# Kernel optimization log

Measured on AMD Instinct MI355X. Metric: run time of the kernel, lower is better.

Reference implementation:

```python
import jax, jax.numpy as jnp
import numpy as np

D_MODEL, N_HEADS, N_LEVELS, N_POINTS = 256, 8, 3, 4
HW = [(100, 152), (50, 76), (25, 38)]
S_TOTAL = sum(h * w for h, w in HW)  # 19950
B = 4


def _bilinear_sample(img, gx, gy, H, W):
    # img: [N, H*W, D]; gx, gy: [N, M] normalized coords in [-1, 1]
    # grid_sample semantics: align_corners=False, padding_mode='zeros'
    ix = (gx + 1.0) * 0.5 * W - 0.5
    iy = (gy + 1.0) * 0.5 * H - 0.5
    x0 = jnp.floor(ix)
    y0 = jnp.floor(iy)
    wx1 = ix - x0
    wy1 = iy - y0

    def corner(xc, yc, w):
        valid = (xc >= 0) & (xc < W) & (yc >= 0) & (yc < H)
        idx = (jnp.clip(yc, 0, H - 1) * W + jnp.clip(xc, 0, W - 1)).astype(jnp.int32)
        vals = jnp.take_along_axis(img, idx[:, :, None], axis=1)  # [N, M, D]
        return vals * (w * valid.astype(img.dtype))[:, :, None]

    return (corner(x0, y0, (1 - wx1) * (1 - wy1))
            + corner(x0 + 1, y0, wx1 * (1 - wy1))
            + corner(x0, y0 + 1, (1 - wx1) * wy1)
            + corner(x0 + 1, y0 + 1, wx1 * wy1))


def setup_inputs() -> dict:
    key = jax.random.key(0)
    ks = jax.random.split(key, 10)
    C = D_MODEL
    sc = 1.0 / np.sqrt(C)
    query = jax.random.normal(ks[0], (B, S_TOTAL, C), jnp.float32)
    value = jax.random.normal(ks[1], (B, S_TOTAL, C), jnp.float32)
    reference_points = jax.random.uniform(ks[2], (B, S_TOTAL, 2), jnp.float32)
    spatial_shapes = np.array(HW, dtype=np.int64)
    sizes = [h * w for h, w in HW]
    level_start_index = np.concatenate([[0], np.cumsum(sizes)[:-1]]).astype(np.int64)
    # Small offset weights keep sampled locations mostly in-bounds (as after training)
    W_off = jax.random.normal(ks[3], (N_HEADS * N_LEVELS * N_POINTS * 2, C), jnp.float32) * 0.01
    b_off = jax.random.normal(ks[4], (N_HEADS * N_LEVELS * N_POINTS * 2,), jnp.float32)
    W_attn = jax.random.normal(ks[5], (N_HEADS * N_LEVELS * N_POINTS, C), jnp.float32) * sc
    b_attn = jnp.zeros((N_HEADS * N_LEVELS * N_POINTS,), jnp.float32)
    W_val = jax.random.normal(ks[6], (C, C), jnp.float32) * sc
    b_val = jnp.zeros((C,), jnp.float32)
    W_out = jax.random.normal(ks[7], (C, C), jnp.float32) * sc
    b_out = jnp.zeros((C,), jnp.float32)
    return {"query": query, "value": value, "spatial_shapes": spatial_shapes,
            "level_start_index": level_start_index, "reference_points": reference_points,
            "W_off": W_off, "b_off": b_off, "W_attn": W_attn, "b_attn": b_attn,
            "W_val": W_val, "b_val": b_val, "W_out": W_out, "b_out": b_out}


def reference(query, value, spatial_shapes, level_start_index, reference_points,
              W_off, b_off, W_attn, b_attn, W_val, b_val, W_out, b_out):
    Bq, S, C = query.shape
    Dh = C // N_HEADS
    ss = np.asarray(spatial_shapes)          # static [L,2] (H,W)
    lsi = np.asarray(level_start_index)      # static [L]

    v = (value @ W_val.T + b_val).reshape(Bq, S, N_HEADS, Dh)
    off = (query @ W_off.T + b_off).reshape(Bq, S, N_HEADS, N_LEVELS, N_POINTS, 2)
    attn = jax.nn.softmax(
        (query @ W_attn.T + b_attn).reshape(Bq, S, N_HEADS, N_LEVELS, N_POINTS), axis=-1)

    # normalizer per level: (W, H) to normalize (x, y) offsets
    normalizer = jnp.asarray(ss[:, ::-1].astype(np.float32))  # [L, 2]
    ref = reference_points[:, :, None, None, None, :]          # [B,S,1,1,1,2]
    loc = ref + off / normalizer[None, None, None, :, None, :]  # [B,S,H,L,P,2]

    out = jnp.zeros((Bq, S, N_HEADS, Dh), query.dtype)
    for lvl in range(N_LEVELS):
        H, W = int(ss[lvl, 0]), int(ss[lvl, 1])
        start = int(lsi[lvl])
        # value for this level: [B*Hn, H*W, Dh]
        v_l = v[:, start:start + H * W].transpose(0, 2, 1, 3).reshape(Bq * N_HEADS, H * W, Dh)
        g = loc[:, :, :, lvl] * 2.0 - 1.0                      # [B,S,Hn,P,2]
        g = g.transpose(0, 2, 1, 3, 4).reshape(Bq * N_HEADS, S * N_POINTS, 2)
        sampled = _bilinear_sample(v_l, g[..., 0], g[..., 1], H, W)  # [B*Hn, S*P, Dh]
        sampled = sampled.reshape(Bq, N_HEADS, S, N_POINTS, Dh)
        w_l = attn[:, :, :, lvl].transpose(0, 2, 1, 3)         # [B,Hn,S,P]
        out = out + jnp.einsum('bhspd,bhsp->bshd', sampled, w_l)
    return out.reshape(Bq, S, C) @ W_out.T + b_out
```

## Files before the change

kernel.cpp:

```cpp
#include <hip/hip_runtime.h>

typedef unsigned short u16;
typedef unsigned int u32;
typedef __attribute__((ext_vector_type(8))) short short8v;
typedef __attribute__((ext_vector_type(4))) float f32x4;
typedef __attribute__((ext_vector_type(2))) float f32x2;
typedef __attribute__((ext_vector_type(4))) unsigned int uint4v;
typedef __attribute__((ext_vector_type(2))) unsigned int uint2v;
typedef __attribute__((ext_vector_type(8))) unsigned short us8;
typedef __attribute__((ext_vector_type(4))) unsigned short us4;

#define B_   4
#define S_   19950
#define C_   256
#define NH   8
#define DH   32
#define BS_  (B_*S_)

#define BM 64
#define BN 128
#define BK 64
#define NPAN 1248

__device__ __forceinline__ float bf2f(u16 u){ u32 x=((u32)u)<<16; float f; __builtin_memcpy(&f,&x,4); return f; }
__device__ __forceinline__ u16 f2bf(float f){ u32 x; __builtin_memcpy(&x,&f,4); x += 0x7fffu + ((x>>16)&1u); return (u16)(x>>16); }
__device__ __forceinline__ u32 cvtpk(float a, float b){ u32 r; asm("v_cvt_pk_bf16_f32 %0, %1, %2" : "=v"(r) : "v"(a), "v"(b)); return r; }
__device__ __forceinline__ f32x2 pkfma(f32x2 a, f32x2 b, f32x2 d){
  asm("v_pk_fma_f32 %0, %1, %2, %0" : "+v"(d) : "v"(a), "v"(b)); return d;
}
__device__ __forceinline__ f32x2 unpk(u32 p){
  uint2v u; u.x = p<<16; u.y = p & 0xffff0000u; return __builtin_bit_cast(f32x2, u);
}

template<int MODE>
__device__ __forceinline__ void gemm_core(int g, u32* smem,
    const void* __restrict__ Aany, const float* __restrict__ Wmain,
    const float* __restrict__ Wattn, const float* __restrict__ bmain,
    const float* __restrict__ battn, void* __restrict__ out0, u16* __restrict__ out1)
{
  constexpr int NX = (MODE==1) ? 3 : 2;
  float* Asf = (float*)smem;
  u16*  Asb  = (u16*)smem;
  u32*  Bs   = smem + ((MODE==2) ? 2048 : 4096);

  const int tid = threadIdx.x;
  const int x = (g>>3) % NX;
  const int y = ((g>>3)/NX)*8 + (g&7);
  const int m0 = y * BM;
  const int n0 = x * BN;
  const int lane = tid & 63;
  const int wid  = tid >> 6;
  const int wm = wid >> 1, wn = wid & 1;
  const int ln15 = lane & 15, ln4 = lane >> 4;

  f32x4 acc[2][4];
  #pragma unroll
  for (int i=0;i<2;++i){
    #pragma unroll
    for (int j=0;j<4;++j) acc[i][j] = (f32x4){0.f,0.f,0.f,0.f};
  }

  f32x4 bvv[8];
  auto loadB = [&](int k0){
    #pragma unroll
    for (int i=0;i<8;++i){
      const int ct = tid + 256*i;
      const int row = ct >> 4, c = ct & 15;
      const int n = n0 + row;
      f32x4 vv = (f32x4){0.f,0.f,0.f,0.f};
      if constexpr (MODE==1) {
        if (n < 192)      vv = *(const f32x4*)(Wmain + (size_t)n*C_ + k0 + c*4);
        else if (n < 288) vv = *(const f32x4*)(Wattn + (size_t)(n-192)*C_ + k0 + c*4);
      } else {
        vv = *(const f32x4*)(Wmain + (size_t)n*C_ + k0 + c*4);
      }
      bvv[i] = vv;
    }
  };

  loadB(0);

  #pragma unroll
  for (int kt=0; kt<4; ++kt) {
    const int k0 = kt*BK;
    if constexpr (MODE==2) {
      const u16* Ab = (const u16*)Aany;
      #pragma unroll
      for (int i=0;i<2;++i){
        const int rl = wid*16 + i*8 + (lane>>3);
        const int rg = min(m0 + rl, BS_-1);
        const int c = lane & 7, cs = c ^ (rl & 7);
        __builtin_amdgcn_global_load_lds(Ab + (size_t)rg*C_ + k0 + cs*8,
            &Asb[(wid*16 + i*8)*64], 16, 0, 0);
      }
    } else {
      const float* Ab = (const float*)Aany;
      #pragma unroll
      for (int i=0;i<4;++i){
        const int rl = wid*16 + i*4 + (lane>>4);
        const int rg = min(m0 + rl, BS_-1);
        const int c = lane & 15, cs = c ^ (rl & 15);
        __builtin_amdgcn_global_load_lds(Ab + (size_t)rg*C_ + k0 + cs*4,
            &Asf[(wid*16 + i*4)*64], 16, 0, 0);
      }
    }
    #pragma unroll
    for (int i=0;i<8;++i){
      const int ct = tid + 256*i;
      const int row = ct >> 4, c = ct & 15;
      const u32 p0 = cvtpk(bvv[i].x, bvv[i].y), p1 = cvtpk(bvv[i].z, bvv[i].w);
      const int cc = c >> 1;
      uint2v pk; pk.x = p0; pk.y = p1;
      *(uint2v*)&Bs[row*32 + ((cc ^ (row&7))<<2) + (c&1)*2] = pk;
    }
    if (kt < 3) loadB(k0 + BK);
    __syncthreads();
    #pragma unroll
    for (int ks=0; ks<2; ++ks) {
      short8v af[2], bfr[4];
      #pragma unroll
      for (int mi=0;mi<2;++mi){
        const int row = wm*32 + mi*16 + ln15;
        if constexpr (MODE==2) {
          const int c = ks*4 + ln4;
          af[mi] = *(const short8v*)&Asb[row*64 + ((c ^ (row&7))<<3)];
        } else {
          const int ch = ks*8 + ln4*2;
          const int c1 = ch ^ (row&15), c2 = (ch+1) ^ (row&15);
          const f32x4 lo = *(const f32x4*)&Asf[row*64 + c1*4];
          const f32x4 hi = *(const f32x4*)&Asf[row*64 + c2*4];
          uint4v uu;
          uu.x = cvtpk(lo.x, lo.y); uu.y = cvtpk(lo.z, lo.w);
          uu.z = cvtpk(hi.x, hi.y); uu.w = cvtpk(hi.z, hi.w);
          af[mi] = __builtin_bit_cast(short8v, uu);
        }
      }
      #pragma unroll
      for (int ni=0;ni<4;++ni){
        const int row = wn*64 + ni*16 + ln15;
        const int c = ks*4 + ln4;
        bfr[ni] = *(const short8v*)&Bs[row*32 + ((c ^ (row&7))<<2)];
      }
      #pragma unroll
      for (int mi=0;mi<2;++mi){
        #pragma unroll
        for (int ni=0;ni<4;++ni)
          acc[mi][ni] = __builtin_amdgcn_mfma_f32_16x16x32_bf16(af[mi], bfr[ni], acc[mi][ni], 0, 0, 0);
      }
    }
    __syncthreads();
  }

  if constexpr (MODE==2) {
    float* Cs = (float*)smem;
    float* outp = (float*)out0;
    #pragma unroll
    for (int p=0;p<2;++p){
      if (wm == p) {
        #pragma unroll
        for (int mi=0;mi<2;++mi){
          #pragma unroll
          for (int ni=0;ni<4;++ni){
            const int col = wn*64 + ni*16 + ln15;
            const float bv = bmain[n0 + col];
            #pragma unroll
            for (int j=0;j<4;++j){
              const int rl = mi*16 + ln4*4 + j;
              Cs[rl*132 + col] = acc[mi][ni][j] + bv;
            }
          }
        }
      }
      __syncthreads();
      #pragma unroll
      for (int i=0;i<4;++i){
        const int c = i*256 + tid;
        const int row = c >> 5, ch = c & 31;
        const int m = m0 + p*32 + row;
        if (m < BS_) {
          const f32x4 vv = *(const f32x4*)&Cs[row*132 + ch*4];
          *(f32x4*)(outp + (size_t)m*C_ + n0 + ch*4) = vv;
        }
      }
      __syncthreads();
    }
  } else {
    u16* Cs = (u16*)smem;
    #pragma unroll
    for (int mi=0;mi<2;++mi){
      #pragma unroll
      for (int ni=0;ni<4;++ni){
        const int col = wn*64 + ni*16 + ln15;
        const int n = n0 + col;
        if (MODE==1 && n >= 288) continue;
        float bias;
        if constexpr (MODE==1) bias = (n < 192) ? bmain[n] : battn[n-192];
        else                   bias = bmain[n];
        if (MODE==1 && n >= 192) {
          #pragma unroll
          for (int j=0;j<4;++j){
            const int row = wm*32 + mi*16 + ln4*4 + j;
            const float vv = acc[mi][ni][j] + bias;
            float mx = vv;
            mx = fmaxf(mx, __shfl_xor(mx, 1));
            mx = fmaxf(mx, __shfl_xor(mx, 2));
            const float e = __expf(vv - mx);
            float ssum = e;
            ssum += __shfl_xor(ssum, 1);
            ssum += __shfl_xor(ssum, 2);
            Cs[row*136 + col] = f2bf(e/ssum);
          }
        } else {
          #pragma unroll
          for (int j=0;j<4;++j){
            const int row = wm*32 + mi*16 + ln4*4 + j;
            Cs[row*136 + col] = f2bf(acc[mi][ni][j] + bias);
          }
        }
      }
    }
    __syncthreads();
    #pragma unroll
    for (int i=0;i<4;++i){
      const int c = i*256 + tid;
      const int row = c >> 4, ch = c & 15;
      const int m = m0 + row;
      if (m >= BS_) continue;
      const int colg = n0 + ch*8;
      const int bq = m / S_, sq = m - bq*S_;
      if constexpr (MODE==0) {
        const uint4v vv = *(const uint4v*)&Cs[row*136 + ch*8];
        u16* vout = (u16*)out0;
        const int h = colg >> 5, dh0 = colg & 31;
        *(uint4v*)(vout + ((size_t)(bq*NH+h)*S_ + sq)*DH + dh0) = vv;
      } else {
        if (colg < 192) {
          const uint4v vv = *(const uint4v*)&Cs[row*136 + ch*8];
          u16* soff = (u16*)out0;
          const int hh = colg / 24, cc = colg - hh*24;
          *(uint4v*)(soff + (((size_t)hh*4 + bq)*S_ + sq)*24 + cc) = vv;
        } else if (colg < 288) {
          #pragma unroll
          for (int half=0; half<2; ++half){
            const int nl2 = colg + half*4 - 192;
            const int hh = nl2 / 12, cc = nl2 - hh*12;
            const uint2v vv = *(const uint2v*)&Cs[row*136 + ch*8 + half*4];
            *(uint2v*)(out1 + (((size_t)hh*4 + bq)*S_ + sq)*12 + cc) = vv;
          }
        }
      }
    }
  }
}

__global__ __launch_bounds__(256) void k_projF(
    const void* __restrict__ value, const float* __restrict__ Wv,
    const float* __restrict__ bv, void* __restrict__ vout,
    const void* __restrict__ query, const float* __restrict__ Wo,
    const float* __restrict__ Wa, const float* __restrict__ bo,
    const float* __restrict__ ba, void* __restrict__ soff, u16* __restrict__ sattn)
{
  __shared__ u32 smem[8192];
  const int g = blockIdx.x;
  if (g < 2*NPAN) gemm_core<0>(g,          smem, value, Wv, nullptr, bv, nullptr, vout, nullptr);
  else            gemm_core<1>(g - 2*NPAN, smem, query, Wo, Wa,      bo, ba,      soff, sattn);
}

__global__ __launch_bounds__(256) void k_gemm2F(const void* __restrict__ A,
    const float* __restrict__ W, const float* __restrict__ b, void* __restrict__ o)
{
  __shared__ u32 smem[6144];
  gemm_core<2>(blockIdx.x, smem, A, W, nullptr, b, nullptr, o, nullptr);
}

#define NCH 312

__global__ __launch_bounds__(256) void k_sample7(const u16* __restrict__ v,
    const u16* __restrict__ soff, const u16* __restrict__ sattn,
    const float* __restrict__ refp, u16* __restrict__ tmp)
{
  const int g = blockIdx.x;
  const int xcd = g & 7, inner = g >> 3;
  const int unit = inner / NCH;
  const int cidx = inner - unit*NCH;
  const int bh = xcd*4 + unit;
  const int b = bh >> 3, h = bh & 7;
  const int dh0 = (threadIdx.x & 3) * 8;
  const int q = cidx*64 + (threadIdx.x >> 2);
  if (q >= S_) return;
  const size_t r = (size_t)b*S_ + q;
  const float refx = refp[r*2+0], refy = refp[r*2+1];
  const char* vb = (const char*)(v + (size_t)bh * S_ * DH);

  const u16* sop = soff + (((size_t)h*4 + b)*S_ + q)*24;
  const u16* sap = sattn + (((size_t)h*4 + b)*S_ + q)*12;
  us8 so0 = *(const us8*)(sop);
  us8 so1 = *(const us8*)(sop + 8);
  us8 so2 = *(const us8*)(sop + 16);
  us4 sa0 = *(const us4*)(sap);
  us4 sa1 = *(const us4*)(sap + 4);
  us4 sa2 = *(const us4*)(sap + 8);
  u16 soarr[24]; u16 saarr[12];
  #pragma unroll
  for (int i=0;i<8;++i){ soarr[i]=so0[i]; soarr[8+i]=so1[i]; soarr[16+i]=so2[i]; }
  #pragma unroll
  for (int i=0;i<4;++i){ saarr[i]=sa0[i]; saarr[4+i]=sa1[i]; saarr[8+i]=sa2[i]; }

  f32x2 acc0 = (f32x2){0.f,0.f}, acc1 = acc0, acc2 = acc0, acc3 = acc0;
  const int WLs[3]={152,76,38}, HLs[3]={100,50,25}, STs[3]={0,15200,19000};
  const u32 ch2 = (u32)(dh0*2);
  #pragma unroll
  for (int l=0;l<3;++l) {
    const int Wl=WLs[l], Hl=HLs[l];
    const float rxl = refx*(float)Wl - 0.5f;
    const float ryl = refy*(float)Hl - 0.5f;
    const char* vbl = vb + (size_t)STs[l]*DH*2;
    #pragma unroll
    for (int p=0;p<4;++p) {
      const int idx = l*4 + p;
      const float ix = rxl + bf2f(soarr[2*idx+0]);
      const float iy = ryl + bf2f(soarr[2*idx+1]);
      const float aw = bf2f(saarr[idx]);
      const float x0f = floorf(ix), y0f = floorf(iy);
      const float wx1 = ix-x0f, wy1 = iy-y0f;
      const int x0 = (int)x0f, y0 = (int)y0f;
      const int x1 = x0+1, y1 = y0+1;
      const float wx0z = ((u32)x0 < (u32)Wl) ? (1.f-wx1) : 0.f;
      const float wx1z = ((u32)x1 < (u32)Wl) ? wx1 : 0.f;
      const float wy0z = ((u32)y0 < (u32)Hl) ? aw*(1.f-wy1) : 0.f;
      const float wy1z = ((u32)y1 < (u32)Hl) ? aw*wy1 : 0.f;
      const int xi0 = min(max(x0,0),Wl-1), xi1 = min(max(x1,0),Wl-1);
      const int yi0 = min(max(y0,0),Hl-1), yi1 = min(max(y1,0),Hl-1);
      const u32 rb0 = (u32)(yi0*Wl)*64u + ch2;
      const u32 rb1 = (u32)(yi1*Wl)*64u + ch2;
      const uint4v t00 = *(const uint4v*)(vbl + rb0 + (u32)xi0*64u);
      const uint4v t01 = *(const uint4v*)(vbl + rb0 + (u32)xi1*64u);
      const uint4v t10 = *(const uint4v*)(vbl + rb1 + (u32)xi0*64u);
      const uint4v t11 = *(const uint4v*)(vbl + rb1 + (u32)xi1*64u);
      const float w00 = wx0z*wy0z, w01 = wx1z*wy0z;
      const float w10 = wx0z*wy1z, w11 = wx1z*wy1z;
      f32x2 W00 = (f32x2){w00,w00}, W01 = (f32x2){w01,w01};
      f32x2 W10 = (f32x2){w10,w10}, W11 = (f32x2){w11,w11};
      acc0 = pkfma(unpk(t00.x), W00, acc0);
      acc1 = pkfma(unpk(t00.y), W00, acc1);
      acc2 = pkfma(unpk(t00.z), W00, acc2);
      acc3 = pkfma(unpk(t00.w), W00, acc3);
      acc0 = pkfma(unpk(t01.x), W01, acc0);
      acc1 = pkfma(unpk(t01.y), W01, acc1);
      acc2 = pkfma(unpk(t01.z), W01, acc2);
      acc3 = pkfma(unpk(t01.w), W01, acc3);
      acc0 = pkfma(unpk(t10.x), W10, acc0);
      acc1 = pkfma(unpk(t10.y), W10, acc1);
      acc2 = pkfma(unpk(t10.z), W10, acc2);
      acc3 = pkfma(unpk(t10.w), W10, acc3);
      acc0 = pkfma(unpk(t11.x), W11, acc0);
      acc1 = pkfma(unpk(t11.y), W11, acc1);
      acc2 = pkfma(unpk(t11.z), W11, acc2);
      acc3 = pkfma(unpk(t11.w), W11, acc3);
    }
  }
  uint4v o;
  o.x = cvtpk(acc0.x, acc0.y); o.y = cvtpk(acc1.x, acc1.y);
  o.z = cvtpk(acc2.x, acc2.y); o.w = cvtpk(acc3.x, acc3.y);
  *(uint4v*)(tmp + r*C_ + (size_t)h*DH + dh0) = o;
}

extern "C" void kernel_launch(void* const* d_in, const int* in_sizes, int n_in,
                              void* d_out, int out_size, void* d_ws, size_t ws_size,
                              hipStream_t stream) {
  (void)in_sizes; (void)n_in; (void)out_size; (void)ws_size;
  const float* query = (const float*)d_in[0];
  const float* value = (const float*)d_in[1];
  const float* refp  = (const float*)d_in[4];
  const float* W_off = (const float*)d_in[5];
  const float* b_off = (const float*)d_in[6];
  const float* W_attn= (const float*)d_in[7];
  const float* b_attn= (const float*)d_in[8];
  const float* W_val = (const float*)d_in[9];
  const float* b_val = (const float*)d_in[10];
  const float* W_out = (const float*)d_in[11];
  const float* b_out = (const float*)d_in[12];
  float* out = (float*)d_out;

  char* ws = (char*)d_ws;
  constexpr size_t V_BYTES    = (size_t)BS_*C_*2;
  constexpr size_t SOFF_BYTES = (size_t)BS_*24*NH*2;
  constexpr size_t SATTN_BYTES= (size_t)BS_*12*NH*2;
  u16* v     = (u16*)(ws);
  u16* soff  = (u16*)(ws + V_BYTES);
  u16* sattn = (u16*)(ws + V_BYTES + SOFF_BYTES);
  u16* tmp   = (u16*)(ws + V_BYTES + SOFF_BYTES + SATTN_BYTES);

  dim3 blk(256);
  hipLaunchKernelGGL(k_projF, dim3(5*NPAN), blk, 0, stream,
                     (const void*)value, W_val, b_val, (void*)v,
                     (const void*)query, W_off, W_attn, b_off, b_attn,
                     (void*)soff, sattn);
  hipLaunchKernelGGL(k_sample7, dim3(8*4*NCH), blk, 0, stream, v, soff, sattn, refp, tmp);
  hipLaunchKernelGGL(k_gemm2F, dim3(2*NPAN), blk, 0, stream,
                     (const void*)tmp, W_out, b_out, (void*)out);
}
```

Measured before the change: 242.1 us.

## Fuse offset and attention-weight projection into the sampling kernel per head

The query projection for sampling offsets and attention logits, including the softmax, moves out of the combined projection kernel and into the sampling kernel. Each block computes its own 64-query by 36-column slice for a single head with bf16 MFMA and keeps the result in shared memory. This removes the global write and re-read of the soff and sattn buffers and shrinks the projection launch to the value GEMM only. In exchange, each query row is read once per head (eight times overall), relying on L2 and the last-level cache to absorb the repeats. The MFMA tiles are also padded from 36 to 48 columns, and the sampling blocks gain a GEMM phase plus extra barriers.

```diff
diff --git a/kernel.cpp b/kernel.cpp
--- a/kernel.cpp
+++ b/kernel.cpp
@@ -35,10 +35,9 @@
 template<int MODE>
 __device__ __forceinline__ void gemm_core(int g, u32* smem,
     const void* __restrict__ Aany, const float* __restrict__ Wmain,
-    const float* __restrict__ Wattn, const float* __restrict__ bmain,
-    const float* __restrict__ battn, void* __restrict__ out0, u16* __restrict__ out1)
+    const float* __restrict__ bmain, void* __restrict__ out0)
 {
-  constexpr int NX = (MODE==1) ? 3 : 2;
+  constexpr int NX = 2;
   float* Asf = (float*)smem;
   u16*  Asb  = (u16*)smem;
   u32*  Bs   = smem + ((MODE==2) ? 2048 : 4096);
@@ -67,14 +66,7 @@
       const int ct = tid + 256*i;
       const int row = ct >> 4, c = ct & 15;
       const int n = n0 + row;
-      f32x4 vv = (f32x4){0.f,0.f,0.f,0.f};
-      if constexpr (MODE==1) {
-        if (n < 192)      vv = *(const f32x4*)(Wmain + (size_t)n*C_ + k0 + c*4);
-        else if (n < 288) vv = *(const f32x4*)(Wattn + (size_t)(n-192)*C_ + k0 + c*4);
-      } else {
-        vv = *(const f32x4*)(Wmain + (size_t)n*C_ + k0 + c*4);
-      }
-      bvv[i] = vv;
+      bvv[i] = *(const f32x4*)(Wmain + (size_t)n*C_ + k0 + c*4);
     }
   };
 
@@ -192,30 +184,11 @@
       for (int ni=0;ni<4;++ni){
         const int col = wn*64 + ni*16 + ln15;
         const int n = n0 + col;
-        if (MODE==1 && n >= 288) continue;
-        float bias;
-        if constexpr (MODE==1) bias = (n < 192) ? bmain[n] : battn[n-192];
-        else                   bias = bmain[n];
-        if (MODE==1 && n >= 192) {
-          #pragma unroll
-          for (int j=0;j<4;++j){
-            const int row = wm*32 + mi*16 + ln4*4 + j;
-            const float vv = acc[mi][ni][j] + bias;
-            float mx = vv;
-            mx = fmaxf(mx, __shfl_xor(mx, 1));
-            mx = fmaxf(mx, __shfl_xor(mx, 2));
-            const float e = __expf(vv - mx);
-            float ssum = e;
-            ssum += __shfl_xor(ssum, 1);
-            ssum += __shfl_xor(ssum, 2);
-            Cs[row*136 + col] = f2bf(e/ssum);
-          }
-        } else {
-          #pragma unroll
-          for (int j=0;j<4;++j){
-            const int row = wm*32 + mi*16 + ln4*4 + j;
-            Cs[row*136 + col] = f2bf(acc[mi][ni][j] + bias);
-          }
+        const float bias = bmain[n];
+        #pragma unroll
+        for (int j=0;j<4;++j){
+          const int row = wm*32 + mi*16 + ln4*4 + j;
+          Cs[row*136 + col] = f2bf(acc[mi][ni][j] + bias);
         }
       }
     }
@@ -228,141 +201,228 @@
       if (m >= BS_) continue;
       const int colg = n0 + ch*8;
       const int bq = m / S_, sq = m - bq*S_;
-      if constexpr (MODE==0) {
-        const uint4v vv = *(const uint4v*)&Cs[row*136 + ch*8];
-        u16* vout = (u16*)out0;
-        const int h = colg >> 5, dh0 = colg & 31;
-        *(uint4v*)(vout + ((size_t)(bq*NH+h)*S_ + sq)*DH + dh0) = vv;
-      } else {
-        if (colg < 192) {
-          const uint4v vv = *(const uint4v*)&Cs[row*136 + ch*8];
-          u16* soff = (u16*)out0;
-          const int hh = colg / 24, cc = colg - hh*24;
-          *(uint4v*)(soff + (((size_t)hh*4 + bq)*S_ + sq)*24 + cc) = vv;
-        } else if (colg < 288) {
-          #pragma unroll
-          for (int half=0; half<2; ++half){
-            const int nl2 = colg + half*4 - 192;
-            const int hh = nl2 / 12, cc = nl2 - hh*12;
-            const uint2v vv = *(const uint2v*)&Cs[row*136 + ch*8 + half*4];
-            *(uint2v*)(out1 + (((size_t)hh*4 + bq)*S_ + sq)*12 + cc) = vv;
-          }
-        }
-      }
+      const uint4v vv = *(const uint4v*)&Cs[row*136 + ch*8];
+      u16* vout = (u16*)out0;
+      const int h = colg >> 5, dh0 = colg & 31;
+      *(uint4v*)(vout + ((size_t)(bq*NH+h)*S_ + sq)*DH + dh0) = vv;
     }
   }
 }
 
 __global__ __launch_bounds__(256) void k_projF(
     const void* __restrict__ value, const float* __restrict__ Wv,
-    const float* __restrict__ bv, void* __restrict__ vout,
-    const void* __restrict__ query, const float* __restrict__ Wo,
-    const float* __restrict__ Wa, const float* __restrict__ bo,
-    const float* __restrict__ ba, void* __restrict__ soff, u16* __restrict__ sattn)
+    const float* __restrict__ bv, void* __restrict__ vout)
 {
   __shared__ u32 smem[8192];
-  const int g = blockIdx.x;
-  if (g < 2*NPAN) gemm_core<0>(g,          smem, value, Wv, nullptr, bv, nullptr, vout, nullptr);
-  else            gemm_core<1>(g - 2*NPAN, smem, query, Wo, Wa,      bo, ba,      soff, sattn);
+  gemm_core<0>(blockIdx.x, smem, value, Wv, bv, vout);
 }
 
 __global__ __launch_bounds__(256) void k_gemm2F(const void* __restrict__ A,
     const float* __restrict__ W, const float* __restrict__ b, void* __restrict__ o)
 {
   __shared__ u32 smem[6144];
-  gemm_core<2>(blockIdx.x, smem, A, W, nullptr, b, nullptr, o, nullptr);
+  gemm_core<2>(blockIdx.x, smem, A, W, b, o);
 }
 
 #define NCH 312
 
-__global__ __launch_bounds__(256) void k_sample7(const u16* __restrict__ v,
-    const u16* __restrict__ soff, const u16* __restrict__ sattn,
+__global__ __launch_bounds__(256) void k_sampleQ(const u16* __restrict__ v,
+    const float* __restrict__ query,
+    const float* __restrict__ W_off, const float* __restrict__ b_off,
+    const float* __restrict__ W_attn, const float* __restrict__ b_attn,
     const float* __restrict__ refp, u16* __restrict__ tmp)
 {
+  __shared__ u32 smem[5632];
+  float* QsF = (float*)smem;
+  u32*  Ws   = smem + 4096;
+  u16*  rec  = (u16*)smem;
+
   const int g = blockIdx.x;
   const int xcd = g & 7, inner = g >> 3;
   const int unit = inner / NCH;
   const int cidx = inner - unit*NCH;
   const int bh = xcd*4 + unit;
   const int b = bh >> 3, h = bh & 7;
-  const int dh0 = (threadIdx.x & 3) * 8;
-  const int q = cidx*64 + (threadIdx.x >> 2);
-  if (q >= S_) return;
-  const size_t r = (size_t)b*S_ + q;
-  const float refx = refp[r*2+0], refy = refp[r*2+1];
-  const char* vb = (const char*)(v + (size_t)bh * S_ * DH);
-
-  const u16* sop = soff + (((size_t)h*4 + b)*S_ + q)*24;
-  const u16* sap = sattn + (((size_t)h*4 + b)*S_ + q)*12;
-  us8 so0 = *(const us8*)(sop);
-  us8 so1 = *(const us8*)(sop + 8);
-  us8 so2 = *(const us8*)(sop + 16);
-  us4 sa0 = *(const us4*)(sap);
-  us4 sa1 = *(const us4*)(sap + 4);
-  us4 sa2 = *(const us4*)(sap + 8);
-  u16 soarr[24]; u16 saarr[12];
+  const int q0 = cidx*64;
+
+  const int tid = threadIdx.x;
+  const int lane = tid & 63;
+  const int wid  = tid >> 6;
+  const int ln15 = lane & 15, ln4 = lane >> 4;
+
+  f32x4 pacc[3];
   #pragma unroll
-  for (int i=0;i<8;++i){ soarr[i]=so0[i]; soarr[8+i]=so1[i]; soarr[16+i]=so2[i]; }
+  for (int i=0;i<3;++i) pacc[i] = (f32x4){0.f,0.f,0.f,0.f};
+
+  f32x4 wv[3];
+  auto loadW = [&](int k0){
+    #pragma unroll
+    for (int i=0;i<3;++i){
+      const int ct = tid + 256*i;
+      const int row = ct >> 4, c = ct & 15;
+      f32x4 vv = (f32x4){0.f,0.f,0.f,0.f};
+      if (row < 24)      vv = *(const f32x4*)(W_off  + (size_t)(h*24+row)*C_ + k0 + c*4);
+      else if (row < 36) vv = *(const f32x4*)(W_attn + (size_t)(h*12+row-24)*C_ + k0 + c*4);
+      wv[i] = vv;
+    }
+  };
+  auto writeW = [&](){
+    #pragma unroll
+    for (int i=0;i<3;++i){
+      const int ct = tid + 256*i;
+      const int row = ct >> 4, c = ct & 15;
+      const u32 p0 = cvtpk(wv[i].x, wv[i].y), p1 = cvtpk(wv[i].z, wv[i].w);
+      const int cc = c >> 1;
+      uint2v pk; pk.x = p0; pk.y = p1;
+      *(uint2v*)&Ws[row*32 + ((cc ^ (row&7))<<2) + (c&1)*2] = pk;
+    }
+  };
+
+  loadW(0);
   #pragma unroll
-  for (int i=0;i<4;++i){ saarr[i]=sa0[i]; saarr[4+i]=sa1[i]; saarr[8+i]=sa2[i]; }
-
-  f32x2 acc0 = (f32x2){0.f,0.f}, acc1 = acc0, acc2 = acc0, acc3 = acc0;
-  const int WLs[3]={152,76,38}, HLs[3]={100,50,25}, STs[3]={0,15200,19000};
-  const u32 ch2 = (u32)(dh0*2);
+  for (int kt=0; kt<4; ++kt){
+    const int k0 = kt*BK;
+    #pragma unroll
+    for (int i=0;i<4;++i){
+      const int rl = wid*16 + i*4 + (lane>>4);
+      const int rg = b*S_ + min(q0 + rl, S_-1);
+      const int c = lane & 15, cs = c ^ (rl & 15);
+      __builtin_amdgcn_global_load_lds(query + (size_t)rg*C_ + k0 + cs*4,
+          &QsF[(wid*16 + i*4)*64], 16, 0, 0);
+    }
+    writeW();
+    if (kt < 3) loadW(k0 + BK);
+    __syncthreads();
+    #pragma unroll
+    for (int ks=0; ks<2; ++ks){
+      const int qrow = wid*16 + ln15;
+      const int ch = ks*8 + ln4*2;
+      const int c1 = ch ^ (qrow&15), c2 = (ch+1) ^ (qrow&15);
+      const f32x4 lo = *(const f32x4*)&QsF[qrow*64 + c1*4];
+      const f32x4 hi = *(const f32x4*)&QsF[qrow*64 + c2*4];
+      uint4v uu;
+      uu.x = cvtpk(lo.x, lo.y); uu.y = cvtpk(lo.z, lo.w);
+      uu.z = cvtpk(hi.x, hi.y); uu.w = cvtpk(hi.z, hi.w);
+      const short8v af = __builtin_bit_cast(short8v, uu);
+      #pragma unroll
+      for (int ni=0;ni<3;++ni){
+        const int wrow = ni*16 + ln15;
+        const int c = ks*4 + ln4;
+        const short8v bfr = *(const short8v*)&Ws[wrow*32 + ((c ^ (wrow&7))<<2)];
+        pacc[ni] = __builtin_amdgcn_mfma_f32_16x16x32_bf16(af, bfr, pacc[ni], 0, 0, 0);
+      }
+    }
+    __syncthreads();
+  }
+
   #pragma unroll
-  for (int l=0;l<3;++l) {
-    const int Wl=WLs[l], Hl=HLs[l];
-    const float rxl = refx*(float)Wl - 0.5f;
-    const float ryl = refy*(float)Hl - 0.5f;
-    const char* vbl = vb + (size_t)STs[l]*DH*2;
-    #pragma unroll
-    for (int p=0;p<4;++p) {
-      const int idx = l*4 + p;
-      const float ix = rxl + bf2f(soarr[2*idx+0]);
-      const float iy = ryl + bf2f(soarr[2*idx+1]);
-      const float aw = bf2f(saarr[idx]);
-      const float x0f = floorf(ix), y0f = floorf(iy);
-      const float wx1 = ix-x0f, wy1 = iy-y0f;
-      const int x0 = (int)x0f, y0 = (int)y0f;
-      const int x1 = x0+1, y1 = y0+1;
-      const float wx0z = ((u32)x0 < (u32)Wl) ? (1.f-wx1) : 0.f;
-      const float wx1z = ((u32)x1 < (u32)Wl) ? wx1 : 0.f;
-      const float wy0z = ((u32)y0 < (u32)Hl) ? aw*(1.f-wy1) : 0.f;
-      const float wy1z = ((u32)y1 < (u32)Hl) ? aw*wy1 : 0.f;
-      const int xi0 = min(max(x0,0),Wl-1), xi1 = min(max(x1,0),Wl-1);
-      const int yi0 = min(max(y0,0),Hl-1), yi1 = min(max(y1,0),Hl-1);
-      const u32 rb0 = (u32)(yi0*Wl)*64u + ch2;
-      const u32 rb1 = (u32)(yi1*Wl)*64u + ch2;
-      const uint4v t00 = *(const uint4v*)(vbl + rb0 + (u32)xi0*64u);
-      const uint4v t01 = *(const uint4v*)(vbl + rb0 + (u32)xi1*64u);
-      const uint4v t10 = *(const uint4v*)(vbl + rb1 + (u32)xi0*64u);
-      const uint4v t11 = *(const uint4v*)(vbl + rb1 + (u32)xi1*64u);
-      const float w00 = wx0z*wy0z, w01 = wx1z*wy0z;
-      const float w10 = wx0z*wy1z, w11 = wx1z*wy1z;
-      f32x2 W00 = (f32x2){w00,w00}, W01 = (f32x2){w01,w01};
-      f32x2 W10 = (f32x2){w10,w10}, W11 = (f32x2){w11,w11};
-      acc0 = pkfma(unpk(t00.x), W00, acc0);
-      acc1 = pkfma(unpk(t00.y), W00, acc1);
-      acc2 = pkfma(unpk(t00.z), W00, acc2);
-      acc3 = pkfma(unpk(t00.w), W00, acc3);
-      acc0 = pkfma(unpk(t01.x), W01, acc0);
-      acc1 = pkfma(unpk(t01.y), W01, acc1);
-      acc2 = pkfma(unpk(t01.z), W01, acc2);
-      acc3 = pkfma(unpk(t01.w), W01, acc3);
-      acc0 = pkfma(unpk(t10.x), W10, acc0);
-      acc1 = pkfma(unpk(t10.y), W10, acc1);
-      acc2 = pkfma(unpk(t10.z), W10, acc2);
-      acc3 = pkfma(unpk(t10.w), W10, acc3);
-      acc0 = pkfma(unpk(t11.x), W11, acc0);
-      acc1 = pkfma(unpk(t11.y), W11, acc1);
-      acc2 = pkfma(unpk(t11.z), W11, acc2);
-      acc3 = pkfma(unpk(t11.w), W11, acc3);
-    }
-  }
-  uint4v o;
-  o.x = cvtpk(acc0.x, acc0.y); o.y = cvtpk(acc1.x, acc1.y);
-  o.z = cvtpk(acc2.x, acc2.y); o.w = cvtpk(acc3.x, acc3.y);
-  *(uint4v*)(tmp + r*C_ + (size_t)h*DH + dh0) = o;
+  for (int ni=0;ni<3;++ni){
+    const int col = ni*16 + ln15;
+    if (col < 24) {
+      const float bv = b_off[h*24 + col];
+      #pragma unroll
+      for (int j=0;j<4;++j){
+        const int qr = wid*16 + ln4*4 + j;
+        rec[qr*40 + col] = f2bf(pacc[ni][j] + bv);
+      }
+    } else if (col < 36) {
+      const float bv = b_attn[h*12 + col - 24];
+      #pragma unroll
+      for (int j=0;j<4;++j){
+        const int qr = wid*16 + ln4*4 + j;
+        const float vv = pacc[ni][j] + bv;
+        float mx = vv;
+        mx = fmaxf(mx, __shfl_xor(mx, 1));
+        mx = fmaxf(mx, __shfl_xor(mx, 2));
+        const float e = __expf(vv - mx);
+        float ssum = e;
+        ssum += __shfl_xor(ssum, 1);
+        ssum += __shfl_xor(ssum, 2);
+        rec[qr*40 + col] = f2bf(e/ssum);
+      }
+    }
+  }
+  __syncthreads();
+
+  const int dh0 = (tid & 3) * 8;
+  const int qloc = tid >> 2;
+  const int q = q0 + qloc;
+  if (q < S_) {
+    const size_t r = (size_t)b*S_ + q;
+    const float refx = refp[r*2+0], refy = refp[r*2+1];
+    const char* vb = (const char*)(v + (size_t)bh * S_ * DH);
+
+    const u16* rp = rec + (size_t)qloc*40;
+    us8 so0 = *(const us8*)(rp);
+    us8 so1 = *(const us8*)(rp + 8);
+    us8 so2 = *(const us8*)(rp + 16);
+    us4 sa0 = *(const us4*)(rp + 24);
+    us4 sa1 = *(const us4*)(rp + 28);
+    us4 sa2 = *(const us4*)(rp + 32);
+    u16 soarr[24]; u16 saarr[12];
+    #pragma unroll
+    for (int i=0;i<8;++i){ soarr[i]=so0[i]; soarr[8+i]=so1[i]; soarr[16+i]=so2[i]; }
+    #pragma unroll
+    for (int i=0;i<4;++i){ saarr[i]=sa0[i]; saarr[4+i]=sa1[i]; saarr[8+i]=sa2[i]; }
+
+    f32x2 acc0 = (f32x2){0.f,0.f}, acc1 = acc0, acc2 = acc0, acc3 = acc0;
+    const int WLs[3]={152,76,38}, HLs[3]={100,50,25}, STs[3]={0,15200,19000};
+    const u32 ch2 = (u32)(dh0*2);
+    #pragma unroll
+    for (int l=0;l<3;++l) {
+      const int Wl=WLs[l], Hl=HLs[l];
+      const float rxl = refx*(float)Wl - 0.5f;
+      const float ryl = refy*(float)Hl - 0.5f;
+      const char* vbl = vb + (size_t)STs[l]*DH*2;
+      #pragma unroll
+      for (int p=0;p<4;++p) {
+        const int idx = l*4 + p;
+        const float ix = rxl + bf2f(soarr[2*idx+0]);
+        const float iy = ryl + bf2f(soarr[2*idx+1]);
+        const float aw = bf2f(saarr[idx]);
+        const float x0f = floorf(ix), y0f = floorf(iy);
+        const float wx1 = ix-x0f, wy1 = iy-y0f;
+        const int x0 = (int)x0f, y0 = (int)y0f;
+        const int x1 = x0+1, y1 = y0+1;
+        const float wx0z = ((u32)x0 < (u32)Wl) ? (1.f-wx1) : 0.f;
+        const float wx1z = ((u32)x1 < (u32)Wl) ? wx1 : 0.f;
+        const float wy0z = ((u32)y0 < (u32)Hl) ? aw*(1.f-wy1) : 0.f;
+        const float wy1z = ((u32)y1 < (u32)Hl) ? aw*wy1 : 0.f;
+        const int xi0 = min(max(x0,0),Wl-1), xi1 = min(max(x1,0),Wl-1);
+        const int yi0 = min(max(y0,0),Hl-1), yi1 = min(max(y1,0),Hl-1);
+        const u32 rb0 = (u32)(yi0*Wl)*64u + ch2;
+        const u32 rb1 = (u32)(yi1*Wl)*64u + ch2;
+        const uint4v t00 = *(const uint4v*)(vbl + rb0 + (u32)xi0*64u);
+        const uint4v t01 = *(const uint4v*)(vbl + rb0 + (u32)xi1*64u);
+        const uint4v t10 = *(const uint4v*)(vbl + rb1 + (u32)xi0*64u);
+        const uint4v t11 = *(const uint4v*)(vbl + rb1 + (u32)xi1*64u);
+        const float w00 = wx0z*wy0z, w01 = wx1z*wy0z;
+        const float w10 = wx0z*wy1z, w11 = wx1z*wy1z;
+        f32x2 W00 = (f32x2){w00,w00}, W01 = (f32x2){w01,w01};
+        f32x2 W10 = (f32x2){w10,w10}, W11 = (f32x2){w11,w11};
+        acc0 = pkfma(unpk(t00.x), W00, acc0);
+        acc1 = pkfma(unpk(t00.y), W00, acc1);
+        acc2 = pkfma(unpk(t00.z), W00, acc2);
+        acc3 = pkfma(unpk(t00.w), W00, acc3);
+        acc0 = pkfma(unpk(t01.x), W01, acc0);
+        acc1 = pkfma(unpk(t01.y), W01, acc1);
+        acc2 = pkfma(unpk(t01.z), W01, acc2);
+        acc3 = pkfma(unpk(t01.w), W01, acc3);
+        acc0 = pkfma(unpk(t10.x), W10, acc0);
+        acc1 = pkfma(unpk(t10.y), W10, acc1);
+        acc2 = pkfma(unpk(t10.z), W10, acc2);
+        acc3 = pkfma(unpk(t10.w), W10, acc3);
+        acc0 = pkfma(unpk(t11.x), W11, acc0);
+        acc1 = pkfma(unpk(t11.y), W11, acc1);
+        acc2 = pkfma(unpk(t11.z), W11, acc2);
+        acc3 = pkfma(unpk(t11.w), W11, acc3);
+      }
+    }
+    uint4v o;
+    o.x = cvtpk(acc0.x, acc0.y); o.y = cvtpk(acc1.x, acc1.y);
+    o.z = cvtpk(acc2.x, acc2.y); o.w = cvtpk(acc3.x, acc3.y);
+    *(uint4v*)(tmp + r*C_ + (size_t)h*DH + dh0) = o;
+  }
 }
 
 extern "C" void kernel_launch(void* const* d_in, const int* in_sizes, int n_in,
@@ -383,20 +443,15 @@
   float* out = (float*)d_out;
 
   char* ws = (char*)d_ws;
-  constexpr size_t V_BYTES    = (size_t)BS_*C_*2;
-  constexpr size_t SOFF_BYTES = (size_t)BS_*24*NH*2;
-  constexpr size_t SATTN_BYTES= (size_t)BS_*12*NH*2;
-  u16* v     = (u16*)(ws);
-  u16* soff  = (u16*)(ws + V_BYTES);
-  u16* sattn = (u16*)(ws + V_BYTES + SOFF_BYTES);
-  u16* tmp   = (u16*)(ws + V_BYTES + SOFF_BYTES + SATTN_BYTES);
+  constexpr size_t V_BYTES = (size_t)BS_*C_*2;
+  u16* v   = (u16*)(ws);
+  u16* tmp = (u16*)(ws + V_BYTES);
 
   dim3 blk(256);
-  hipLaunchKernelGGL(k_projF, dim3(5*NPAN), blk, 0, stream,
-                     (const void*)value, W_val, b_val, (void*)v,
-                     (const void*)query, W_off, W_attn, b_off, b_attn,
-                     (void*)soff, sattn);
-  hipLaunchKernelGGL(k_sample7, dim3(8*4*NCH), blk, 0, stream, v, soff, sattn, refp, tmp);
+  hipLaunchKernelGGL(k_projF, dim3(2*NPAN), blk, 0, stream,
+                     (const void*)value, W_val, b_val, (void*)v);
+  hipLaunchKernelGGL(k_sampleQ, dim3(8*4*NCH), blk, 0, stream,
+                     v, query, W_off, b_off, W_attn, b_attn, refp, tmp);
   hipLaunchKernelGGL(k_gemm2F, dim3(2*NPAN), blk, 0, stream,
                      (const void*)tmp, W_out, b_out, (void*)out);
 }
```

Result: no change. 245.3 us (+1.3%).
